# Kernel tuning notes

Measured on AMD Instinct MI355X. Metric: run time of the kernel, lower is better.

## Reference

```python
import jax, jax.numpy as jnp
import numpy as np

N_HEADS, N_LEVELS, N_POINTS = 8, 4, 4


def _sample_bilinear(feat_flat, H, W, x, y):
    """feat_flat: [B, H*W, nH, hd]; x,y: [B,Q,nH,P] pixel coords (align_corners=False).
    Zero padding outside. Returns [B,Q,nH,P,hd]."""
    x0 = jnp.floor(x); y0 = jnp.floor(y)
    wx = x - x0; wy = y - y0                       # bilinear weights
    x0i = x0.astype(jnp.int32); y0i = y0.astype(jnp.int32)

    def gather(ix, iy):
        valid = ((ix >= 0) & (ix < W) & (iy >= 0) & (iy < H)).astype(feat_flat.dtype)
        idx = jnp.clip(iy, 0, H - 1) * W + jnp.clip(ix, 0, W - 1)
        B, Q, nH, P = idx.shape
        hd = feat_flat.shape[-1]
        idx2 = idx.transpose(0, 1, 3, 2).reshape(B, Q * P, nH)[..., None]
        v = jnp.take_along_axis(feat_flat, idx2, axis=1)       # [B,Q*P,nH,hd]
        v = v.reshape(B, Q, P, nH, hd).transpose(0, 1, 3, 2, 4)  # [B,Q,nH,P,hd]
        return v * valid[..., None]

    v00 = gather(x0i, y0i); v01 = gather(x0i + 1, y0i)
    v10 = gather(x0i, y0i + 1); v11 = gather(x0i + 1, y0i + 1)
    wxe = wx[..., None]; wye = wy[..., None]
    return (v00 * (1 - wxe) + v01 * wxe) * (1 - wye) + (v10 * (1 - wxe) + v11 * wxe) * wye


def setup_inputs() -> dict:
    key = jax.random.key(0)
    ks = jax.random.split(key, 10)
    B, C = 2, 256
    shapes = np.array([[128, 128], [64, 64], [32, 32], [16, 16]], dtype=np.int64)
    lens = shapes[:, 0] * shapes[:, 1]
    Len = int(lens.sum())  # 21760
    lsi = np.concatenate([[0], np.cumsum(lens)[:-1]])
    return {
        "query": jax.random.normal(ks[0], (B, Len, C), jnp.float32),
        "reference_points": jax.random.uniform(ks[1], (B, Len, 2), dtype=jnp.float32),
        "input_flatten": jax.random.normal(ks[2], (B, Len, C), jnp.float32),
        "spatial_shapes": jnp.asarray(shapes),
        "level_start_index": jnp.asarray(lsi),
        "W_off": jax.random.normal(ks[3], (C, N_HEADS * N_LEVELS * N_POINTS * 2), jnp.float32) * 0.01,
        "b_off": jax.random.normal(ks[4], (N_HEADS * N_LEVELS * N_POINTS * 2,), jnp.float32) * 0.01,
        "W_attn": jax.random.normal(ks[5], (C, N_HEADS * N_LEVELS * N_POINTS), jnp.float32) * 0.02,
        "b_attn": jax.random.normal(ks[6], (N_HEADS * N_LEVELS * N_POINTS,), jnp.float32) * 0.02,
        "W_out": jax.random.normal(ks[7], (C, C), jnp.float32) * 0.02,
        "b_out": jax.random.normal(ks[8], (C,), jnp.float32) * 0.02,
    }


def reference(query, reference_points, input_flatten, spatial_shapes, level_start_index,
              W_off, b_off, W_attn, b_attn, W_out, b_out):
    B, Q, C = query.shape
    nH, nL, nP = N_HEADS, N_LEVELS, N_POINTS
    hd = C // nH

    off = (query @ W_off + b_off).reshape(B, Q, nH, nL, nP, 2)
    aw = jax.nn.softmax((query @ W_attn + b_attn).reshape(B, Q, nH, nL * nP), axis=-1)
    aw = aw.reshape(B, Q, nH, nL, nP)

    shapes = np.asarray(spatial_shapes)                     # static (H,W) per level
    normalizer = jnp.asarray(np.stack([shapes[:, 1], shapes[:, 0]], -1), query.dtype)  # (W,H)
    loc = reference_points[:, :, None, None, None, :] + off / normalizer[None, None, None, :, None, :]

    starts = np.concatenate([[0], np.cumsum(shapes[:, 0] * shapes[:, 1])])
    out = jnp.zeros((B, Q, nH, hd), query.dtype)
    for lvl in range(nL):
        H, W = int(shapes[lvl, 0]), int(shapes[lvl, 1])
        feat = input_flatten[:, int(starts[lvl]):int(starts[lvl + 1]), :].reshape(B, H * W, nH, hd)
        l = loc[:, :, :, lvl, :, :]                          # [B,Q,nH,P,2]
        # grid_sample align_corners=False: pixel = ((2*loc-1)+1)/2*size - 0.5 = loc*size - 0.5
        x = l[..., 0] * W - 0.5
        y = l[..., 1] * H - 0.5
        sampled = _sample_bilinear(feat, H, W, x, y)         # [B,Q,nH,P,hd]
        out = out + (sampled * aw[:, :, :, lvl, :, None]).sum(axis=3)

    return out.reshape(B, Q, C) @ W_out + b_out
```

## Files before the change

kernel.cpp:

```cpp
#include <hip/hip_runtime.h>


#define NH 8
#define NL 4
#define NP 4
#define CDIM 256
#define HD 32
#define QB 16

typedef short bf16x8 __attribute__((ext_vector_type(8)));
typedef float f32x4  __attribute__((ext_vector_type(4)));
typedef _Float16 f16x8v __attribute__((ext_vector_type(8)));
typedef _Float16 f16x4v __attribute__((ext_vector_type(4)));

#define SPLAT8(x) (f16x8v){(x),(x),(x),(x),(x),(x),(x),(x)}

__device__ __forceinline__ short f2bf(float x) {
    union { float f; unsigned u; } v; v.f = x;
    const unsigned r = v.u + 0x7FFFu + ((v.u >> 16) & 1u);
    return (short)(r >> 16);
}
__device__ __forceinline__ float bf2f(short s) {
    union { unsigned u; float f; } v; v.u = ((unsigned)(unsigned short)s) << 16;
    return v.f;
}

__constant__ int LVL_S_C[4] = {0, 16384, 20480, 21504};

__global__ __launch_bounds__(256) void convert_w(
    const float* __restrict__ W_off, const float* __restrict__ W_attn,
    const float* __restrict__ W_out, short* __restrict__ wt)
{
    const int gid = blockIdx.x * 256 + threadIdx.x;
    if (gid < 65536) {
        const int c = gid >> 8, k = gid & 255;
        wt[gid] = f2bf(W_off[k * 256 + c]);
    } else if (gid < 98304) {
        const int g = gid - 65536, c = g >> 8, k = g & 255;
        wt[gid] = f2bf(W_attn[k * 128 + c]);
    } else if (gid < 163840) {
        const int g = gid - 98304, c = g >> 8, k = g & 255;
        wt[gid] = f2bf(W_out[k * 256 + c]);
    }
}

__global__ __launch_bounds__(256) void convert_feat_f16(
    const float* __restrict__ feat, _Float16* __restrict__ fh, int n4)
{
    const int gid = blockIdx.x * 256 + threadIdx.x;
    if (gid < n4) {
        const float4 v = *(const float4*)&feat[gid * 4];
        f16x4v o;
        o[0] = (_Float16)v.x; o[1] = (_Float16)v.y;
        o[2] = (_Float16)v.z; o[3] = (_Float16)v.w;
        *(f16x4v*)&fh[gid * 4] = o;
    }
}

__global__ __launch_bounds__(256) void gemm1_kernel(
    const float* __restrict__ query, const short* __restrict__ wt,
    const float* __restrict__ b_off, const float* __restrict__ b_attn,
    float* __restrict__ offs_g, float* __restrict__ aw_g)
{
    const int t = threadIdx.x;
    const int lane = t & 63;
    const int wave = t >> 6;
    const int qr = lane & 15;
    const int quad = lane >> 4;
    const long long qbase = (long long)blockIdx.x * QB;

    __shared__ __align__(16) short qp[QB * CDIM];

    #pragma unroll
    for (int it = 0; it < 4; ++it) {
        const int e = it * 1024 + t * 4;
        const int i = e >> 8, k = e & 255;
        const float4 v = *(const float4*)&query[(qbase + i) * CDIM + k];
        const int chunk = (k >> 5) * 64 + ((k >> 3) & 3) * 16 + i;
        short4 o;
        o.x = f2bf(v.x); o.y = f2bf(v.y); o.z = f2bf(v.z); o.w = f2bf(v.w);
        *(short4*)&qp[chunk * 8 + (k & 7)] = o;
    }
    __syncthreads();

    const short* __restrict__ Wt_off  = wt;
    const short* __restrict__ Wt_attn = wt + 65536;

    f32x4 acc[4], acca[2];
    #pragma unroll
    for (int j = 0; j < 4; ++j) acc[j] = (f32x4){0.f, 0.f, 0.f, 0.f};
    #pragma unroll
    for (int j = 0; j < 2; ++j) acca[j] = (f32x4){0.f, 0.f, 0.f, 0.f};

    const short* bb_off  = Wt_off  + qr * 256 + quad * 8;
    const short* bb_attn = Wt_attn + qr * 256 + quad * 8;
    #pragma unroll
    for (int s = 0; s < 8; ++s) {
        const bf16x8 af = *(const bf16x8*)&qp[(s * 64 + lane) * 8];
        #pragma unroll
        for (int j = 0; j < 4; ++j) {
            const bf16x8 bf = *(const bf16x8*)(bb_off + ((j * 4 + wave) * 16) * 256 + s * 32);
            acc[j] = __builtin_amdgcn_mfma_f32_16x16x32_bf16(af, bf, acc[j], 0, 0, 0);
        }
        #pragma unroll
        for (int j = 0; j < 2; ++j) {
            const bf16x8 bf = *(const bf16x8*)(bb_attn + ((j * 4 + wave) * 16) * 256 + s * 32);
            acca[j] = __builtin_amdgcn_mfma_f32_16x16x32_bf16(af, bf, acca[j], 0, 0, 0);
        }
    }
    #pragma unroll
    for (int j = 0; j < 4; ++j) {
        const int col = (j * 4 + wave) * 16 + qr;
        const float bo = b_off[col];
        #pragma unroll
        for (int r = 0; r < 4; ++r)
            offs_g[(qbase + quad * 4 + r) * 256 + col] = acc[j][r] + bo;
    }
    #pragma unroll
    for (int j = 0; j < 2; ++j) {
        const int col = (j * 4 + wave) * 16 + qr;
        const float ba = b_attn[col];
        #pragma unroll
        for (int r = 0; r < 4; ++r)
            aw_g[(qbase + quad * 4 + r) * 128 + col] = acca[j][r] + ba;
    }
}

__global__ __launch_bounds__(256) void sampler_kernel(
    const float* __restrict__ ref_pts, const _Float16* __restrict__ featfh,
    const float* __restrict__ offs_g, const float* __restrict__ aw_g,
    short* __restrict__ pre_g, int Len)
{
    const int t = threadIdx.x;
    const int rl = t >> 5;
    const int l32 = t & 31;
    const int h = l32 >> 2, ct = l32 & 3;
    const int row = blockIdx.x * 8 + rl;
    const int b = row / Len;

    const float rx = ref_pts[row * 2];
    const float ry = ref_pts[row * 2 + 1];
    const float* __restrict__ offr = offs_g + (long long)row * 256 + h * 32;
    const float* __restrict__ awr  = aw_g  + (long long)row * 128 + h * 16;

    float mxv = -1e30f;
    #pragma unroll
    for (int j = 0; j < 16; ++j) mxv = fmaxf(mxv, awr[j]);
    float ssum = 0.f;
    #pragma unroll
    for (int j = 0; j < 16; ++j) ssum += __expf(awr[j] - mxv);
    const float inv = 1.f / ssum;

    const int c0 = h * HD + ct * 8;
    float acc[8];
    #pragma unroll
    for (int c = 0; c < 8; ++c) acc[c] = 0.f;

    #pragma unroll
    for (int l = 0; l < NL; ++l) {
        const int Wl = 128 >> l;
        const int base = (b * Len + LVL_S_C[l]) * CDIM + c0;
        #pragma unroll
        for (int p = 0; p < NP; ++p) {
            const int pi = l * 4 + p;
            const float ox = offr[pi * 2];
            const float oy = offr[pi * 2 + 1];
            const float a  = __expf(awr[pi] - mxv) * inv;
            const float x = fmaf(rx, (float)Wl, ox) - 0.5f;
            const float y = fmaf(ry, (float)Wl, oy) - 0.5f;
            const float xf = floorf(x), yf = floorf(y);
            const int x0 = (int)xf, y0 = (int)yf;
            const float wx = x - xf, wy = y - yf;
            const float ax0 = ((unsigned)x0     < (unsigned)Wl) ? (1.f - wx) : 0.f;
            const float ax1 = ((unsigned)(x0+1) < (unsigned)Wl) ? wx         : 0.f;
            const float ay0 = (((unsigned)y0     < (unsigned)Wl) ? (1.f - wy) : 0.f) * a;
            const float ay1 = (((unsigned)(y0+1) < (unsigned)Wl) ? wy         : 0.f) * a;
            const int x0c = min(max(x0, 0), Wl - 1), x1c = min(max(x0 + 1, 0), Wl - 1);
            const int y0c = min(max(y0, 0), Wl - 1), y1c = min(max(y0 + 1, 0), Wl - 1);
            const int r00 = base + (y0c * Wl + x0c) * CDIM;
            const int r01 = base + (y0c * Wl + x1c) * CDIM;
            const int r10 = base + (y1c * Wl + x0c) * CDIM;
            const int r11 = base + (y1c * Wl + x1c) * CDIM;
            const f16x8v v00 = *(const f16x8v*)(featfh + r00);
            const f16x8v v01 = *(const f16x8v*)(featfh + r01);
            const f16x8v v10 = *(const f16x8v*)(featfh + r10);
            const f16x8v v11 = *(const f16x8v*)(featfh + r11);
            const f16x8v W00 = SPLAT8((_Float16)(ax0 * ay0));
            const f16x8v W01 = SPLAT8((_Float16)(ax1 * ay0));
            const f16x8v W10 = SPLAT8((_Float16)(ax0 * ay1));
            const f16x8v W11 = SPLAT8((_Float16)(ax1 * ay1));
            const f16x8v bil = v00 * W00 + v01 * W01 + v10 * W10 + v11 * W11;
            #pragma unroll
            for (int c = 0; c < 8; ++c) acc[c] += (float)bil[c];
        }
    }
    bf16x8 pv;
    #pragma unroll
    for (int c = 0; c < 8; ++c) pv[c] = f2bf(acc[c]);
    *(bf16x8*)&pre_g[(long long)(row >> 4) * 4096 + (h * 64 + ct * 16 + (row & 15)) * 8] = pv;
}

__global__ __launch_bounds__(256) void gemm2_kernel(
    const short* __restrict__ pre_g, const short* __restrict__ wt,
    const float* __restrict__ b_out, float* __restrict__ out)
{
    const int t = threadIdx.x;
    const int lane = t & 63;
    const int wave = t >> 6;
    const int qr = lane & 15;
    const int quad = lane >> 4;
    const long long qbase = (long long)blockIdx.x * QB;
    const short* __restrict__ ap = pre_g + (long long)blockIdx.x * 4096;
    const short* __restrict__ Wt_out = wt + 98304;

    f32x4 acc[4];
    #pragma unroll
    for (int j = 0; j < 4; ++j) acc[j] = (f32x4){0.f, 0.f, 0.f, 0.f};
    const short* bb = Wt_out + qr * 256 + quad * 8;
    #pragma unroll
    for (int s = 0; s < 8; ++s) {
        const bf16x8 af = *(const bf16x8*)&ap[(s * 64 + lane) * 8];
        #pragma unroll
        for (int j = 0; j < 4; ++j) {
            const bf16x8 bf = *(const bf16x8*)(bb + ((j * 4 + wave) * 16) * 256 + s * 32);
            acc[j] = __builtin_amdgcn_mfma_f32_16x16x32_bf16(af, bf, acc[j], 0, 0, 0);
        }
    }
    #pragma unroll
    for (int j = 0; j < 4; ++j) {
        const int col = (j * 4 + wave) * 16 + qr;
        const float bo = b_out[col];
        #pragma unroll
        for (int r = 0; r < 4; ++r)
            out[(qbase + quad * 4 + r) * CDIM + col] = acc[j][r] + bo;
    }
}

__global__ __launch_bounds__(256) void msda_fused_fb(
    const float* __restrict__ query, const float* __restrict__ ref_pts,
    const float* __restrict__ feat_f32, const short* __restrict__ wt,
    const float* __restrict__ b_off, const float* __restrict__ b_attn,
    const float* __restrict__ b_out, float* __restrict__ out, int Len)
{
    const int t = threadIdx.x;
    const int lane = t & 63;
    const int wave = t >> 6;
    const int qr = lane & 15;
    const int quad = lane >> 4;
    const long long qbase = (long long)blockIdx.x * QB;
    const int b = (int)(qbase / Len);

    __shared__ __align__(16) char uni[QB * CDIM * 4];
    short* qp = (short*)uni;
    float* offs_sm = (float*)uni;
    __shared__ float aw_sm[QB][NH * NL * NP + 4];
    __shared__ __align__(16) short pre_pack[QB * CDIM];
    __shared__ float ref_sm[QB][2];

    #pragma unroll
    for (int it = 0; it < 4; ++it) {
        const int e = it * 1024 + t * 4;
        const int i = e >> 8, k = e & 255;
        const float4 v = *(const float4*)&query[(qbase + i) * CDIM + k];
        const int chunk = (k >> 5) * 64 + ((k >> 3) & 3) * 16 + i;
        short4 o;
        o.x = f2bf(v.x); o.y = f2bf(v.y); o.z = f2bf(v.z); o.w = f2bf(v.w);
        *(short4*)&qp[chunk * 8 + (k & 7)] = o;
    }
    if (t < QB * 2) ref_sm[t >> 1][t & 1] = ref_pts[(qbase + (t >> 1)) * 2 + (t & 1)];
    __syncthreads();

    const short* __restrict__ Wt_off  = wt;
    const short* __restrict__ Wt_attn = wt + 65536;
    const short* __restrict__ Wt_out  = wt + 98304;

    {
        f32x4 acc[4], acca[2];
        #pragma unroll
        for (int j = 0; j < 4; ++j) acc[j] = (f32x4){0.f, 0.f, 0.f, 0.f};
        #pragma unroll
        for (int j = 0; j < 2; ++j) acca[j] = (f32x4){0.f, 0.f, 0.f, 0.f};
        const short* bb_off  = Wt_off  + qr * 256 + quad * 8;
        const short* bb_attn = Wt_attn + qr * 256 + quad * 8;
        #pragma unroll
        for (int s = 0; s < 8; ++s) {
            const bf16x8 af = *(const bf16x8*)&qp[(s * 64 + lane) * 8];
            #pragma unroll
            for (int j = 0; j < 4; ++j) {
                const bf16x8 bf = *(const bf16x8*)(bb_off + ((j * 4 + wave) * 16) * 256 + s * 32);
                acc[j] = __builtin_amdgcn_mfma_f32_16x16x32_bf16(af, bf, acc[j], 0, 0, 0);
            }
            #pragma unroll
            for (int j = 0; j < 2; ++j) {
                const bf16x8 bf = *(const bf16x8*)(bb_attn + ((j * 4 + wave) * 16) * 256 + s * 32);
                acca[j] = __builtin_amdgcn_mfma_f32_16x16x32_bf16(af, bf, acca[j], 0, 0, 0);
            }
        }
        __syncthreads();
        #pragma unroll
        for (int j = 0; j < 4; ++j) {
            const int col = (j * 4 + wave) * 16 + qr;
            const float bo = b_off[col];
            const int hh = col >> 5, rem = col & 31;
            #pragma unroll
            for (int r = 0; r < 4; ++r)
                offs_sm[(quad * 4 + r) * 256 + rem * 8 + hh] = acc[j][r] + bo;
        }
        #pragma unroll
        for (int j = 0; j < 2; ++j) {
            const int col = (j * 4 + wave) * 16 + qr;
            const float ba = b_attn[col];
            const int hh = col >> 4, rem = col & 15;
            #pragma unroll
            for (int r = 0; r < 4; ++r)
                aw_sm[quad * 4 + r][rem * 8 + hh] = acca[j][r] + ba;
        }
    }
    __syncthreads();

    if (t < QB * NH) {
        const int i = t >> 3, hh = t & 7;
        float vals[16], mx = -1e30f;
        #pragma unroll
        for (int j = 0; j < 16; ++j) { vals[j] = aw_sm[i][j * 8 + hh]; mx = fmaxf(mx, vals[j]); }
        float s = 0.f;
        #pragma unroll
        for (int j = 0; j < 16; ++j) { vals[j] = __expf(vals[j] - mx); s += vals[j]; }
        const float inv = 1.f / s;
        #pragma unroll
        for (int j = 0; j < 16; ++j) aw_sm[i][j * 8 + hh] = vals[j] * inv;
    }
    __syncthreads();

    {
        const int q2 = lane >> 5;
        const int hh = (lane >> 2) & 7;
        const int ct = lane & 3;
        const int c0 = hh * HD + ct * 8;
        #pragma unroll 1
        for (int it = 0; it < 2; ++it) {
            const int i = wave * 4 + it * 2 + q2;
            const float rx = ref_sm[i][0], ry = ref_sm[i][1];
            float acc[8];
            #pragma unroll
            for (int c = 0; c < 8; ++c) acc[c] = 0.f;
            #pragma unroll
            for (int l = 0; l < NL; ++l) {
                const int Wl = 128 >> l;
                const int base = (b * Len + LVL_S_C[l]) * CDIM + c0;
                #pragma unroll 2
                for (int p = 0; p < NP; ++p) {
                    const int pi = l * 4 + p;
                    const float ox = offs_sm[i * 256 + (pi * 2) * 8 + hh];
                    const float oy = offs_sm[i * 256 + (pi * 2 + 1) * 8 + hh];
                    const float a  = aw_sm[i][pi * 8 + hh];
                    const float x = fmaf(rx, (float)Wl, ox) - 0.5f;
                    const float y = fmaf(ry, (float)Wl, oy) - 0.5f;
                    const float xf = floorf(x), yf = floorf(y);
                    const int x0 = (int)xf, y0 = (int)yf;
                    const float wx = x - xf, wy = y - yf;
                    const float ax0 = ((unsigned)x0     < (unsigned)Wl) ? (1.f - wx) : 0.f;
                    const float ax1 = ((unsigned)(x0+1) < (unsigned)Wl) ? wx         : 0.f;
                    const float ay0 = (((unsigned)y0     < (unsigned)Wl) ? (1.f - wy) : 0.f) * a;
                    const float ay1 = (((unsigned)(y0+1) < (unsigned)Wl) ? wy         : 0.f) * a;
                    const int x0c = min(max(x0, 0), Wl - 1), x1c = min(max(x0 + 1, 0), Wl - 1);
                    const int y0c = min(max(y0, 0), Wl - 1), y1c = min(max(y0 + 1, 0), Wl - 1);
                    const float w00 = ax0 * ay0, w01 = ax1 * ay0;
                    const float w10 = ax0 * ay1, w11 = ax1 * ay1;
                    const int r0 = base + (y0c * Wl + x0c) * CDIM;
                    const int r1 = base + (y0c * Wl + x1c) * CDIM;
                    const int r2 = base + (y1c * Wl + x0c) * CDIM;
                    const int r3 = base + (y1c * Wl + x1c) * CDIM;
                    f32x4 a0 = *(const f32x4*)(feat_f32 + r0);
                    f32x4 a1 = *(const f32x4*)(feat_f32 + r0 + 4);
                    f32x4 b0 = *(const f32x4*)(feat_f32 + r1);
                    f32x4 b1 = *(const f32x4*)(feat_f32 + r1 + 4);
                    f32x4 c0v = *(const f32x4*)(feat_f32 + r2);
                    f32x4 c1 = *(const f32x4*)(feat_f32 + r2 + 4);
                    f32x4 d0 = *(const f32x4*)(feat_f32 + r3);
                    f32x4 d1 = *(const f32x4*)(feat_f32 + r3 + 4);
                    #pragma unroll
                    for (int c = 0; c < 4; ++c) {
                        acc[c]     += w00*a0[c] + w01*b0[c] + w10*c0v[c] + w11*d0[c];
                        acc[c + 4] += w00*a1[c] + w01*b1[c] + w10*c1[c]  + w11*d1[c];
                    }
                }
            }
            bf16x8 pv;
            #pragma unroll
            for (int c = 0; c < 8; ++c) pv[c] = f2bf(acc[c]);
            *(bf16x8*)&pre_pack[(hh * 64 + ct * 16 + i) * 8] = pv;
        }
    }
    __syncthreads();

    {
        f32x4 acc[4];
        #pragma unroll
        for (int j = 0; j < 4; ++j) acc[j] = (f32x4){0.f, 0.f, 0.f, 0.f};
        const short* bb = Wt_out + qr * 256 + quad * 8;
        #pragma unroll
        for (int s = 0; s < 8; ++s) {
            const bf16x8 af = *(const bf16x8*)&pre_pack[(s * 64 + lane) * 8];
            #pragma unroll
            for (int j = 0; j < 4; ++j) {
                const bf16x8 bf = *(const bf16x8*)(bb + ((j * 4 + wave) * 16) * 256 + s * 32);
                acc[j] = __builtin_amdgcn_mfma_f32_16x16x32_bf16(af, bf, acc[j], 0, 0, 0);
            }
        }
        #pragma unroll
        for (int j = 0; j < 4; ++j) {
            const int col = (j * 4 + wave) * 16 + qr;
            const float bo = b_out[col];
            #pragma unroll
            for (int r = 0; r < 4; ++r)
                out[(qbase + quad * 4 + r) * CDIM + col] = acc[j][r] + bo;
        }
    }
}

extern "C" void kernel_launch(void* const* d_in, const int* in_sizes, int n_in,
                              void* d_out, int out_size, void* d_ws, size_t ws_size,
                              hipStream_t stream) {
    const float* query   = (const float*)d_in[0];
    const float* ref_pts = (const float*)d_in[1];
    const float* feat    = (const float*)d_in[2];
    const float* W_off  = (const float*)d_in[5];
    const float* b_off  = (const float*)d_in[6];
    const float* W_attn = (const float*)d_in[7];
    const float* b_attn = (const float*)d_in[8];
    const float* W_out  = (const float*)d_in[9];
    const float* b_out  = (const float*)d_in[10];
    float* out = (float*)d_out;

    const int B = 2;
    const int Len = in_sizes[1] / (B * 2);
    const int rows = B * Len;
    const size_t feat_elems = (size_t)rows * CDIM;

    const size_t off_wt     = 0;
    const size_t off_feath  = 327680;
    const size_t off_offs   = off_feath + feat_elems * 2;
    const size_t off_aw     = off_offs + (size_t)rows * 256 * 4;
    const size_t off_pre    = off_aw + (size_t)rows * 128 * 4;
    const size_t need_full  = off_pre + (size_t)rows * 256 * 2;

    char* ws = (char*)d_ws;
    short* wt = (short*)(ws + off_wt);

    convert_w<<<640, 256, 0, stream>>>(W_off, W_attn, W_out, wt);

    if (ws_size >= need_full) {
        _Float16* feath = (_Float16*)(ws + off_feath);
        float* offs_g = (float*)(ws + off_offs);
        float* aw_g   = (float*)(ws + off_aw);
        short* pre_g  = (short*)(ws + off_pre);
        const int n4 = (int)(feat_elems / 4);
        convert_feat_f16<<<(n4 + 255) / 256, 256, 0, stream>>>(feat, feath, n4);
        gemm1_kernel<<<rows / QB, 256, 0, stream>>>(query, wt, b_off, b_attn, offs_g, aw_g);
        sampler_kernel<<<rows / 8, 256, 0, stream>>>(ref_pts, feath, offs_g, aw_g, pre_g, Len);
        gemm2_kernel<<<rows / QB, 256, 0, stream>>>(pre_g, wt, b_out, out);
    } else {
        msda_fused_fb<<<rows / QB, 256, 0, stream>>>(query, ref_pts, feat, wt,
                                                     b_off, b_attn, b_out, out, Len);
    }
}
```

Before: 337.8 us.

## Fuse projection GEMM, sampler and output GEMM into one kernel

Replaces the separate gemm1, sampler and gemm2 kernels with one kernel per 16-query tile. Offsets, attention weights and the sampled pre-projection values now stay in padded LDS buffers instead of making global round trips, and the softmax is computed once per head in shared memory. The weight and feature conversion kernels are merged into one launch. In exchange, each block uses more LDS and does less work per launch in the sampling phase, which may reduce occupancy.

Measured after the change: 374.5 us. 1.11x slower.

```diff
diff --git a/kernel.cpp b/kernel.cpp
--- a/kernel.cpp
+++ b/kernel.cpp
@@ -7,6 +7,8 @@
 #define CDIM 256
 #define HD 32
 #define QB 16
+#define QSTR 264
+#define ASTR 132
 
 typedef short bf16x8 __attribute__((ext_vector_type(8)));
 typedef float f32x4  __attribute__((ext_vector_type(4)));
@@ -20,47 +22,44 @@
     const unsigned r = v.u + 0x7FFFu + ((v.u >> 16) & 1u);
     return (short)(r >> 16);
 }
-__device__ __forceinline__ float bf2f(short s) {
-    union { unsigned u; float f; } v; v.u = ((unsigned)(unsigned short)s) << 16;
-    return v.f;
+
+__constant__ int LVL_S_C[4] = {0, 16384, 20480, 21504};
+
+__global__ __launch_bounds__(256) void convert_all(
+    const float* __restrict__ W_off, const float* __restrict__ W_attn,
+    const float* __restrict__ W_out, const float* __restrict__ feat,
+    short* __restrict__ wt, _Float16* __restrict__ fh, int n4)
+{
+    const int bid = blockIdx.x;
+    if (bid < 640) {
+        const int gid = bid * 256 + threadIdx.x;
+        if (gid < 65536) {
+            const int c = gid >> 8, k = gid & 255;
+            wt[gid] = f2bf(W_off[k * 256 + c]);
+        } else if (gid < 98304) {
+            const int g = gid - 65536, c = g >> 8, k = g & 255;
+            wt[gid] = f2bf(W_attn[k * 128 + c]);
+        } else if (gid < 163840) {
+            const int g = gid - 98304, c = g >> 8, k = g & 255;
+            wt[gid] = f2bf(W_out[k * 256 + c]);
+        }
+    } else {
+        const int gid = (bid - 640) * 256 + threadIdx.x;
+        if (gid < n4) {
+            const float4 v = *(const float4*)&feat[gid * 4];
+            f16x4v o;
+            o[0] = (_Float16)v.x; o[1] = (_Float16)v.y;
+            o[2] = (_Float16)v.z; o[3] = (_Float16)v.w;
+            *(f16x4v*)&fh[gid * 4] = o;
+        }
+    }
 }
 
-__constant__ int LVL_S_C[4] = {0, 16384, 20480, 21504};
-
-__global__ __launch_bounds__(256) void convert_w(
-    const float* __restrict__ W_off, const float* __restrict__ W_attn,
-    const float* __restrict__ W_out, short* __restrict__ wt)
-{
-    const int gid = blockIdx.x * 256 + threadIdx.x;
-    if (gid < 65536) {
-        const int c = gid >> 8, k = gid & 255;
-        wt[gid] = f2bf(W_off[k * 256 + c]);
-    } else if (gid < 98304) {
-        const int g = gid - 65536, c = g >> 8, k = g & 255;
-        wt[gid] = f2bf(W_attn[k * 128 + c]);
-    } else if (gid < 163840) {
-        const int g = gid - 98304, c = g >> 8, k = g & 255;
-        wt[gid] = f2bf(W_out[k * 256 + c]);
-    }
-}
-
-__global__ __launch_bounds__(256) void convert_feat_f16(
-    const float* __restrict__ feat, _Float16* __restrict__ fh, int n4)
-{
-    const int gid = blockIdx.x * 256 + threadIdx.x;
-    if (gid < n4) {
-        const float4 v = *(const float4*)&feat[gid * 4];
-        f16x4v o;
-        o[0] = (_Float16)v.x; o[1] = (_Float16)v.y;
-        o[2] = (_Float16)v.z; o[3] = (_Float16)v.w;
-        *(f16x4v*)&fh[gid * 4] = o;
-    }
-}
-
-__global__ __launch_bounds__(256) void gemm1_kernel(
-    const float* __restrict__ query, const short* __restrict__ wt,
+__global__ __launch_bounds__(256) void msda_mega(
+    const float* __restrict__ query, const float* __restrict__ ref_pts,
+    const _Float16* __restrict__ feath, const short* __restrict__ wt,
     const float* __restrict__ b_off, const float* __restrict__ b_attn,
-    float* __restrict__ offs_g, float* __restrict__ aw_g)
+    const float* __restrict__ b_out, float* __restrict__ out, int Len)
 {
     const int t = threadIdx.x;
     const int lane = t & 63;
@@ -68,171 +67,174 @@
     const int qr = lane & 15;
     const int quad = lane >> 4;
     const long long qbase = (long long)blockIdx.x * QB;
-
-    __shared__ __align__(16) short qp[QB * CDIM];
+    const int b = (int)(qbase / Len);
+
+    __shared__ __align__(16) char uni[QB * QSTR * 4];
+    short* qp = (short*)uni;
+    float* offs_lds = (float*)uni;
+    __shared__ float aw_lds[QB * ASTR];
+    __shared__ __align__(16) short pre_lds[QB * QSTR];
+    __shared__ float ref_sm[QB][2];
 
     #pragma unroll
     for (int it = 0; it < 4; ++it) {
         const int e = it * 1024 + t * 4;
         const int i = e >> 8, k = e & 255;
         const float4 v = *(const float4*)&query[(qbase + i) * CDIM + k];
-        const int chunk = (k >> 5) * 64 + ((k >> 3) & 3) * 16 + i;
         short4 o;
         o.x = f2bf(v.x); o.y = f2bf(v.y); o.z = f2bf(v.z); o.w = f2bf(v.w);
-        *(short4*)&qp[chunk * 8 + (k & 7)] = o;
-    }
+        *(short4*)&qp[i * QSTR + k] = o;
+    }
+    if (t < QB * 2) ref_sm[t >> 1][t & 1] = ref_pts[(qbase + (t >> 1)) * 2 + (t & 1)];
     __syncthreads();
 
     const short* __restrict__ Wt_off  = wt;
     const short* __restrict__ Wt_attn = wt + 65536;
-
-    f32x4 acc[4], acca[2];
-    #pragma unroll
-    for (int j = 0; j < 4; ++j) acc[j] = (f32x4){0.f, 0.f, 0.f, 0.f};
-    #pragma unroll
-    for (int j = 0; j < 2; ++j) acca[j] = (f32x4){0.f, 0.f, 0.f, 0.f};
-
-    const short* bb_off  = Wt_off  + qr * 256 + quad * 8;
-    const short* bb_attn = Wt_attn + qr * 256 + quad * 8;
-    #pragma unroll
-    for (int s = 0; s < 8; ++s) {
-        const bf16x8 af = *(const bf16x8*)&qp[(s * 64 + lane) * 8];
+    const short* __restrict__ Wt_out  = wt + 98304;
+
+    {
+        f32x4 acc[4], acca[2];
+        #pragma unroll
+        for (int j = 0; j < 4; ++j) acc[j] = (f32x4){0.f, 0.f, 0.f, 0.f};
+        #pragma unroll
+        for (int j = 0; j < 2; ++j) acca[j] = (f32x4){0.f, 0.f, 0.f, 0.f};
+
+        const short* bb_off  = Wt_off  + qr * 256 + quad * 8;
+        const short* bb_attn = Wt_attn + qr * 256 + quad * 8;
+        #pragma unroll
+        for (int s = 0; s < 8; ++s) {
+            const bf16x8 af = *(const bf16x8*)&qp[qr * QSTR + s * 32 + quad * 8];
+            #pragma unroll
+            for (int j = 0; j < 4; ++j) {
+                const bf16x8 bf = *(const bf16x8*)(bb_off + ((j * 4 + wave) * 16) * 256 + s * 32);
+                acc[j] = __builtin_amdgcn_mfma_f32_16x16x32_bf16(af, bf, acc[j], 0, 0, 0);
+            }
+            #pragma unroll
+            for (int j = 0; j < 2; ++j) {
+                const bf16x8 bf = *(const bf16x8*)(bb_attn + ((j * 4 + wave) * 16) * 256 + s * 32);
+                acca[j] = __builtin_amdgcn_mfma_f32_16x16x32_bf16(af, bf, acca[j], 0, 0, 0);
+            }
+        }
+        __syncthreads();
+
         #pragma unroll
         for (int j = 0; j < 4; ++j) {
-            const bf16x8 bf = *(const bf16x8*)(bb_off + ((j * 4 + wave) * 16) * 256 + s * 32);
-            acc[j] = __builtin_amdgcn_mfma_f32_16x16x32_bf16(af, bf, acc[j], 0, 0, 0);
+            const int col = (j * 4 + wave) * 16 + qr;
+            const float bo = b_off[col];
+            const int h = col >> 5, rem = col & 31;
+            #pragma unroll
+            for (int r = 0; r < 4; ++r)
+                offs_lds[(quad * 4 + r) * QSTR + rem * 8 + h] = acc[j][r] + bo;
         }
         #pragma unroll
         for (int j = 0; j < 2; ++j) {
-            const bf16x8 bf = *(const bf16x8*)(bb_attn + ((j * 4 + wave) * 16) * 256 + s * 32);
-            acca[j] = __builtin_amdgcn_mfma_f32_16x16x32_bf16(af, bf, acca[j], 0, 0, 0);
-        }
-    }
-    #pragma unroll
-    for (int j = 0; j < 4; ++j) {
-        const int col = (j * 4 + wave) * 16 + qr;
-        const float bo = b_off[col];
-        #pragma unroll
-        for (int r = 0; r < 4; ++r)
-            offs_g[(qbase + quad * 4 + r) * 256 + col] = acc[j][r] + bo;
-    }
-    #pragma unroll
-    for (int j = 0; j < 2; ++j) {
-        const int col = (j * 4 + wave) * 16 + qr;
-        const float ba = b_attn[col];
-        #pragma unroll
-        for (int r = 0; r < 4; ++r)
-            aw_g[(qbase + quad * 4 + r) * 128 + col] = acca[j][r] + ba;
-    }
-}
-
-__global__ __launch_bounds__(256) void sampler_kernel(
-    const float* __restrict__ ref_pts, const _Float16* __restrict__ featfh,
-    const float* __restrict__ offs_g, const float* __restrict__ aw_g,
-    short* __restrict__ pre_g, int Len)
-{
-    const int t = threadIdx.x;
-    const int rl = t >> 5;
-    const int l32 = t & 31;
-    const int h = l32 >> 2, ct = l32 & 3;
-    const int row = blockIdx.x * 8 + rl;
-    const int b = row / Len;
-
-    const float rx = ref_pts[row * 2];
-    const float ry = ref_pts[row * 2 + 1];
-    const float* __restrict__ offr = offs_g + (long long)row * 256 + h * 32;
-    const float* __restrict__ awr  = aw_g  + (long long)row * 128 + h * 16;
-
-    float mxv = -1e30f;
-    #pragma unroll
-    for (int j = 0; j < 16; ++j) mxv = fmaxf(mxv, awr[j]);
-    float ssum = 0.f;
-    #pragma unroll
-    for (int j = 0; j < 16; ++j) ssum += __expf(awr[j] - mxv);
-    const float inv = 1.f / ssum;
-
-    const int c0 = h * HD + ct * 8;
-    float acc[8];
-    #pragma unroll
-    for (int c = 0; c < 8; ++c) acc[c] = 0.f;
-
-    #pragma unroll
-    for (int l = 0; l < NL; ++l) {
-        const int Wl = 128 >> l;
-        const int base = (b * Len + LVL_S_C[l]) * CDIM + c0;
-        #pragma unroll
-        for (int p = 0; p < NP; ++p) {
-            const int pi = l * 4 + p;
-            const float ox = offr[pi * 2];
-            const float oy = offr[pi * 2 + 1];
-            const float a  = __expf(awr[pi] - mxv) * inv;
-            const float x = fmaf(rx, (float)Wl, ox) - 0.5f;
-            const float y = fmaf(ry, (float)Wl, oy) - 0.5f;
-            const float xf = floorf(x), yf = floorf(y);
-            const int x0 = (int)xf, y0 = (int)yf;
-            const float wx = x - xf, wy = y - yf;
-            const float ax0 = ((unsigned)x0     < (unsigned)Wl) ? (1.f - wx) : 0.f;
-            const float ax1 = ((unsigned)(x0+1) < (unsigned)Wl) ? wx         : 0.f;
-            const float ay0 = (((unsigned)y0     < (unsigned)Wl) ? (1.f - wy) : 0.f) * a;
-            const float ay1 = (((unsigned)(y0+1) < (unsigned)Wl) ? wy         : 0.f) * a;
-            const int x0c = min(max(x0, 0), Wl - 1), x1c = min(max(x0 + 1, 0), Wl - 1);
-            const int y0c = min(max(y0, 0), Wl - 1), y1c = min(max(y0 + 1, 0), Wl - 1);
-            const int r00 = base + (y0c * Wl + x0c) * CDIM;
-            const int r01 = base + (y0c * Wl + x1c) * CDIM;
-            const int r10 = base + (y1c * Wl + x0c) * CDIM;
-            const int r11 = base + (y1c * Wl + x1c) * CDIM;
-            const f16x8v v00 = *(const f16x8v*)(featfh + r00);
-            const f16x8v v01 = *(const f16x8v*)(featfh + r01);
-            const f16x8v v10 = *(const f16x8v*)(featfh + r10);
-            const f16x8v v11 = *(const f16x8v*)(featfh + r11);
-            const f16x8v W00 = SPLAT8((_Float16)(ax0 * ay0));
-            const f16x8v W01 = SPLAT8((_Float16)(ax1 * ay0));
-            const f16x8v W10 = SPLAT8((_Float16)(ax0 * ay1));
-            const f16x8v W11 = SPLAT8((_Float16)(ax1 * ay1));
-            const f16x8v bil = v00 * W00 + v01 * W01 + v10 * W10 + v11 * W11;
-            #pragma unroll
-            for (int c = 0; c < 8; ++c) acc[c] += (float)bil[c];
-        }
-    }
-    bf16x8 pv;
-    #pragma unroll
-    for (int c = 0; c < 8; ++c) pv[c] = f2bf(acc[c]);
-    *(bf16x8*)&pre_g[(long long)(row >> 4) * 4096 + (h * 64 + ct * 16 + (row & 15)) * 8] = pv;
-}
-
-__global__ __launch_bounds__(256) void gemm2_kernel(
-    const short* __restrict__ pre_g, const short* __restrict__ wt,
-    const float* __restrict__ b_out, float* __restrict__ out)
-{
-    const int t = threadIdx.x;
-    const int lane = t & 63;
-    const int wave = t >> 6;
-    const int qr = lane & 15;
-    const int quad = lane >> 4;
-    const long long qbase = (long long)blockIdx.x * QB;
-    const short* __restrict__ ap = pre_g + (long long)blockIdx.x * 4096;
-    const short* __restrict__ Wt_out = wt + 98304;
-
-    f32x4 acc[4];
-    #pragma unroll
-    for (int j = 0; j < 4; ++j) acc[j] = (f32x4){0.f, 0.f, 0.f, 0.f};
-    const short* bb = Wt_out + qr * 256 + quad * 8;
-    #pragma unroll
-    for (int s = 0; s < 8; ++s) {
-        const bf16x8 af = *(const bf16x8*)&ap[(s * 64 + lane) * 8];
+            const int col = (j * 4 + wave) * 16 + qr;
+            const float ba = b_attn[col];
+            const int h = col >> 4, rem = col & 15;
+            #pragma unroll
+            for (int r = 0; r < 4; ++r)
+                aw_lds[(quad * 4 + r) * ASTR + rem * 8 + h] = acca[j][r] + ba;
+        }
+    }
+    __syncthreads();
+
+    if (t < QB * NH) {
+        const int i = t >> 3, h = t & 7;
+        float* row = &aw_lds[i * ASTR];
+        float vals[16], mx = -1e30f;
+        #pragma unroll
+        for (int j = 0; j < 16; ++j) { vals[j] = row[j * 8 + h]; mx = fmaxf(mx, vals[j]); }
+        float s = 0.f;
+        #pragma unroll
+        for (int j = 0; j < 16; ++j) { vals[j] = __expf(vals[j] - mx); s += vals[j]; }
+        const float inv = 1.f / s;
+        #pragma unroll
+        for (int j = 0; j < 16; ++j) row[j * 8 + h] = vals[j] * inv;
+    }
+    __syncthreads();
+
+    {
+        const int rl = t >> 5;
+        const int l32 = t & 31;
+        const int h = l32 >> 2, ct = l32 & 3;
+        const int c0 = h * HD + ct * 8;
+        #pragma unroll 1
+        for (int pass = 0; pass < 2; ++pass) {
+            const int i = pass * 8 + rl;
+            const float rx = ref_sm[i][0], ry = ref_sm[i][1];
+            const float* __restrict__ offr = &offs_lds[i * QSTR];
+            const float* __restrict__ awr  = &aw_lds[i * ASTR];
+            float acc[8];
+            #pragma unroll
+            for (int c = 0; c < 8; ++c) acc[c] = 0.f;
+            #pragma unroll
+            for (int l = 0; l < NL; ++l) {
+                const int Wl = 128 >> l;
+                const int base = (b * Len + LVL_S_C[l]) * CDIM + c0;
+                #pragma unroll
+                for (int p = 0; p < NP; ++p) {
+                    const int pi = l * 4 + p;
+                    const float ox = offr[pi * 16 + h];
+                    const float oy = offr[pi * 16 + 8 + h];
+                    const float a  = awr[pi * 8 + h];
+                    const float x = fmaf(rx, (float)Wl, ox) - 0.5f;
+                    const float y = fmaf(ry, (float)Wl, oy) - 0.5f;
+                    const float xf = floorf(x), yf = floorf(y);
+                    const int x0 = (int)xf, y0 = (int)yf;
+                    const float wx = x - xf, wy = y - yf;
+                    const float ax0 = ((unsigned)x0     < (unsigned)Wl) ? (1.f - wx) : 0.f;
+                    const float ax1 = ((unsigned)(x0+1) < (unsigned)Wl) ? wx         : 0.f;
+                    const float ay0 = (((unsigned)y0     < (unsigned)Wl) ? (1.f - wy) : 0.f) * a;
+                    const float ay1 = (((unsigned)(y0+1) < (unsigned)Wl) ? wy         : 0.f) * a;
+                    const int x0c = min(max(x0, 0), Wl - 1), x1c = min(max(x0 + 1, 0), Wl - 1);
+                    const int y0c = min(max(y0, 0), Wl - 1), y1c = min(max(y0 + 1, 0), Wl - 1);
+                    const int r00 = base + (y0c * Wl + x0c) * CDIM;
+                    const int r01 = base + (y0c * Wl + x1c) * CDIM;
+                    const int r10 = base + (y1c * Wl + x0c) * CDIM;
+                    const int r11 = base + (y1c * Wl + x1c) * CDIM;
+                    const f16x8v v00 = *(const f16x8v*)(feath + r00);
+                    const f16x8v v01 = *(const f16x8v*)(feath + r01);
+                    const f16x8v v10 = *(const f16x8v*)(feath + r10);
+                    const f16x8v v11 = *(const f16x8v*)(feath + r11);
+                    const f16x8v W00 = SPLAT8((_Float16)(ax0 * ay0));
+                    const f16x8v W01 = SPLAT8((_Float16)(ax1 * ay0));
+                    const f16x8v W10 = SPLAT8((_Float16)(ax0 * ay1));
+                    const f16x8v W11 = SPLAT8((_Float16)(ax1 * ay1));
+                    const f16x8v bil = v00 * W00 + v01 * W01 + v10 * W10 + v11 * W11;
+                    #pragma unroll
+                    for (int c = 0; c < 8; ++c) acc[c] += (float)bil[c];
+                }
+            }
+            bf16x8 pv;
+            #pragma unroll
+            for (int c = 0; c < 8; ++c) pv[c] = f2bf(acc[c]);
+            *(bf16x8*)&pre_lds[i * QSTR + c0] = pv;
+        }
+    }
+    __syncthreads();
+
+    {
+        f32x4 acc[4];
+        #pragma unroll
+        for (int j = 0; j < 4; ++j) acc[j] = (f32x4){0.f, 0.f, 0.f, 0.f};
+        const short* bb = Wt_out + qr * 256 + quad * 8;
+        #pragma unroll
+        for (int s = 0; s < 8; ++s) {
+            const bf16x8 af = *(const bf16x8*)&pre_lds[qr * QSTR + s * 32 + quad * 8];
+            #pragma unroll
+            for (int j = 0; j < 4; ++j) {
+                const bf16x8 bf = *(const bf16x8*)(bb + ((j * 4 + wave) * 16) * 256 + s * 32);
+                acc[j] = __builtin_amdgcn_mfma_f32_16x16x32_bf16(af, bf, acc[j], 0, 0, 0);
+            }
+        }
         #pragma unroll
         for (int j = 0; j < 4; ++j) {
-            const bf16x8 bf = *(const bf16x8*)(bb + ((j * 4 + wave) * 16) * 256 + s * 32);
-            acc[j] = __builtin_amdgcn_mfma_f32_16x16x32_bf16(af, bf, acc[j], 0, 0, 0);
-        }
-    }
-    #pragma unroll
-    for (int j = 0; j < 4; ++j) {
-        const int col = (j * 4 + wave) * 16 + qr;
-        const float bo = b_out[col];
-        #pragma unroll
-        for (int r = 0; r < 4; ++r)
-            out[(qbase + quad * 4 + r) * CDIM + col] = acc[j][r] + bo;
+            const int col = (j * 4 + wave) * 16 + qr;
+            const float bo = b_out[col];
+            #pragma unroll
+            for (int r = 0; r < 4; ++r)
+                out[(qbase + quad * 4 + r) * CDIM + col] = acc[j][r] + bo;
+        }
     }
 }
 
@@ -250,11 +252,11 @@
     const long long qbase = (long long)blockIdx.x * QB;
     const int b = (int)(qbase / Len);
 
-    __shared__ __align__(16) char uni[QB * CDIM * 4];
+    __shared__ __align__(16) char uni[QB * QSTR * 4];
     short* qp = (short*)uni;
-    float* offs_sm = (float*)uni;
-    __shared__ float aw_sm[QB][NH * NL * NP + 4];
-    __shared__ __align__(16) short pre_pack[QB * CDIM];
+    float* offs_lds = (float*)uni;
+    __shared__ float aw_lds[QB * ASTR];
+    __shared__ __align__(16) short pre_lds[QB * QSTR];
     __shared__ float ref_sm[QB][2];
 
     #pragma unroll
@@ -262,10 +264,9 @@
         const int e = it * 1024 + t * 4;
         const int i = e >> 8, k = e & 255;
         const float4 v = *(const float4*)&query[(qbase + i) * CDIM + k];
-        const int chunk = (k >> 5) * 64 + ((k >> 3) & 3) * 16 + i;
         short4 o;
         o.x = f2bf(v.x); o.y = f2bf(v.y); o.z = f2bf(v.z); o.w = f2bf(v.w);
-        *(short4*)&qp[chunk * 8 + (k & 7)] = o;
+        *(short4*)&qp[i * QSTR + k] = o;
     }
     if (t < QB * 2) ref_sm[t >> 1][t & 1] = ref_pts[(qbase + (t >> 1)) * 2 + (t & 1)];
     __syncthreads();
@@ -284,7 +285,7 @@
         const short* bb_attn = Wt_attn + qr * 256 + quad * 8;
         #pragma unroll
         for (int s = 0; s < 8; ++s) {
-            const bf16x8 af = *(const bf16x8*)&qp[(s * 64 + lane) * 8];
+            const bf16x8 af = *(const bf16x8*)&qp[qr * QSTR + s * 32 + quad * 8];
             #pragma unroll
             for (int j = 0; j < 4; ++j) {
                 const bf16x8 bf = *(const bf16x8*)(bb_off + ((j * 4 + wave) * 16) * 256 + s * 32);
@@ -301,46 +302,49 @@
         for (int j = 0; j < 4; ++j) {
             const int col = (j * 4 + wave) * 16 + qr;
             const float bo = b_off[col];
-            const int hh = col >> 5, rem = col & 31;
-            #pragma unroll
-            for (int r = 0; r < 4; ++r)
-                offs_sm[(quad * 4 + r) * 256 + rem * 8 + hh] = acc[j][r] + bo;
+            const int h = col >> 5, rem = col & 31;
+            #pragma unroll
+            for (int r = 0; r < 4; ++r)
+                offs_lds[(quad * 4 + r) * QSTR + rem * 8 + h] = acc[j][r] + bo;
         }
         #pragma unroll
         for (int j = 0; j < 2; ++j) {
             const int col = (j * 4 + wave) * 16 + qr;
             const float ba = b_attn[col];
-            const int hh = col >> 4, rem = col & 15;
-            #pragma unroll
-            for (int r = 0; r < 4; ++r)
-                aw_sm[quad * 4 + r][rem * 8 + hh] = acca[j][r] + ba;
+            const int h = col >> 4, rem = col & 15;
+            #pragma unroll
+            for (int r = 0; r < 4; ++r)
+                aw_lds[(quad * 4 + r) * ASTR + rem * 8 + h] = acca[j][r] + ba;
         }
     }
     __syncthreads();
 
     if (t < QB * NH) {
-        const int i = t >> 3, hh = t & 7;
+        const int i = t >> 3, h = t & 7;
+        float* row = &aw_lds[i * ASTR];
         float vals[16], mx = -1e30f;
         #pragma unroll
-        for (int j = 0; j < 16; ++j) { vals[j] = aw_sm[i][j * 8 + hh]; mx = fmaxf(mx, vals[j]); }
+        for (int j = 0; j < 16; ++j) { vals[j] = row[j * 8 + h]; mx = fmaxf(mx, vals[j]); }
         float s = 0.f;
         #pragma unroll
         for (int j = 0; j < 16; ++j) { vals[j] = __expf(vals[j] - mx); s += vals[j]; }
         const float inv = 1.f / s;
         #pragma unroll
-        for (int j = 0; j < 16; ++j) aw_sm[i][j * 8 + hh] = vals[j] * inv;
-    }
-    __syncthreads();
-
-    {
-        const int q2 = lane >> 5;
-        const int hh = (lane >> 2) & 7;
-        const int ct = lane & 3;
-        const int c0 = hh * HD + ct * 8;
+        for (int j = 0; j < 16; ++j) row[j * 8 + h] = vals[j] * inv;
+    }
+    __syncthreads();
+
+    {
+        const int rl = t >> 5;
+        const int l32 = t & 31;
+        const int h = l32 >> 2, ct = l32 & 3;
+        const int c0 = h * HD + ct * 8;
         #pragma unroll 1
-        for (int it = 0; it < 2; ++it) {
-            const int i = wave * 4 + it * 2 + q2;
+        for (int pass = 0; pass < 2; ++pass) {
+            const int i = pass * 8 + rl;
             const float rx = ref_sm[i][0], ry = ref_sm[i][1];
+            const float* __restrict__ offr = &offs_lds[i * QSTR];
+            const float* __restrict__ awr  = &aw_lds[i * ASTR];
             float acc[8];
             #pragma unroll
             for (int c = 0; c < 8; ++c) acc[c] = 0.f;
@@ -351,9 +355,9 @@
                 #pragma unroll 2
                 for (int p = 0; p < NP; ++p) {
                     const int pi = l * 4 + p;
-                    const float ox = offs_sm[i * 256 + (pi * 2) * 8 + hh];
-                    const float oy = offs_sm[i * 256 + (pi * 2 + 1) * 8 + hh];
-                    const float a  = aw_sm[i][pi * 8 + hh];
+                    const float ox = offr[pi * 16 + h];
+                    const float oy = offr[pi * 16 + 8 + h];
+                    const float a  = awr[pi * 8 + h];
                     const float x = fmaf(rx, (float)Wl, ox) - 0.5f;
                     const float y = fmaf(ry, (float)Wl, oy) - 0.5f;
                     const float xf = floorf(x), yf = floorf(y);
@@ -389,7 +393,7 @@
             bf16x8 pv;
             #pragma unroll
             for (int c = 0; c < 8; ++c) pv[c] = f2bf(acc[c]);
-            *(bf16x8*)&pre_pack[(hh * 64 + ct * 16 + i) * 8] = pv;
+            *(bf16x8*)&pre_lds[i * QSTR + c0] = pv;
         }
     }
     __syncthreads();
@@ -401,7 +405,7 @@
         const short* bb = Wt_out + qr * 256 + quad * 8;
         #pragma unroll
         for (int s = 0; s < 8; ++s) {
-            const bf16x8 af = *(const bf16x8*)&pre_pack[(s * 64 + lane) * 8];
+            const bf16x8 af = *(const bf16x8*)&pre_lds[qr * QSTR + s * 32 + quad * 8];
             #pragma unroll
             for (int j = 0; j < 4; ++j) {
                 const bf16x8 bf = *(const bf16x8*)(bb + ((j * 4 + wave) * 16) * 256 + s * 32);
@@ -438,29 +442,21 @@
     const int rows = B * Len;
     const size_t feat_elems = (size_t)rows * CDIM;
 
-    const size_t off_wt     = 0;
-    const size_t off_feath  = 327680;
-    const size_t off_offs   = off_feath + feat_elems * 2;
-    const size_t off_aw     = off_offs + (size_t)rows * 256 * 4;
-    const size_t off_pre    = off_aw + (size_t)rows * 128 * 4;
-    const size_t need_full  = off_pre + (size_t)rows * 256 * 2;
-
     char* ws = (char*)d_ws;
-    short* wt = (short*)(ws + off_wt);
-
-    convert_w<<<640, 256, 0, stream>>>(W_off, W_attn, W_out, wt);
-
-    if (ws_size >= need_full) {
-        _Float16* feath = (_Float16*)(ws + off_feath);
-        float* offs_g = (float*)(ws + off_offs);
-        float* aw_g   = (float*)(ws + off_aw);
-        short* pre_g  = (short*)(ws + off_pre);
+    short* wt = (short*)ws;
+    _Float16* feath = (_Float16*)(ws + 327680);
+    const size_t need = 327680 + feat_elems * 2;
+
+    if (ws_size >= need) {
         const int n4 = (int)(feat_elems / 4);
-        convert_feat_f16<<<(n4 + 255) / 256, 256, 0, stream>>>(feat, feath, n4);
-        gemm1_kernel<<<rows / QB, 256, 0, stream>>>(query, wt, b_off, b_attn, offs_g, aw_g);
-        sampler_kernel<<<rows / 8, 256, 0, stream>>>(ref_pts, feath, offs_g, aw_g, pre_g, Len);
-        gemm2_kernel<<<rows / QB, 256, 0, stream>>>(pre_g, wt, b_out, out);
+        const int fblocks = (n4 + 255) / 256;
+        convert_all<<<640 + fblocks, 256, 0, stream>>>(W_off, W_attn, W_out, feat,
+                                                       wt, feath, n4);
+        msda_mega<<<rows / QB, 256, 0, stream>>>(query, ref_pts, feath, wt,
+                                                 b_off, b_attn, b_out, out, Len);
     } else {
+        convert_all<<<640, 256, 0, stream>>>(W_off, W_attn, W_out, feat,
+                                             wt, (_Float16*)nullptr, 0);
         msda_fused_fb<<<rows / QB, 256, 0, stream>>>(query, ref_pts, feat, wt,
                                                      b_off, b_attn, b_out, out, Len);
     }
```
